# Kernel optimization log

Measured on AMD Instinct MI355X. Metric: run time of the kernel, lower is better.

Reference implementation:

```python
import jax, jax.numpy as jnp
import numpy as np

EPS = 1e-5

def mean_variance_norm(x):
    # x: [b,c,h,w]; torch .var(dim=2) on flattened spatial is UNBIASED (n-1)
    b, c, h, w = x.shape
    n = h * w
    mean = jnp.mean(x, axis=(2, 3), keepdims=True)
    var = jnp.sum((x - mean) ** 2, axis=(2, 3), keepdims=True) / (n - 1) + EPS
    return (x - mean) / jnp.sqrt(var)

def conv1x1(x, W, b):
    # 1x1 conv == channel-mixing matmul. W: [out_c, in_c], b: [out_c]
    return jnp.einsum('oc,bchw->bohw', W, x) + b[None, :, None, None]

def setup_inputs() -> dict:
    key = jax.random.key(0)
    ks = jax.random.split(key, 10)
    C = 512
    shp = (4, C, 64, 64)
    std = 1.0 / np.sqrt(C)
    return {
        'content': jax.random.normal(ks[0], shp, jnp.float32),
        'style': jax.random.normal(ks[1], shp, jnp.float32),
        'Wf': jax.random.normal(ks[2], (C, C), jnp.float32) * std,
        'bf': jax.random.normal(ks[3], (C,), jnp.float32) * 0.01,
        'Wg': jax.random.normal(ks[4], (C, C), jnp.float32) * std,
        'bg': jax.random.normal(ks[5], (C,), jnp.float32) * 0.01,
        'Wh': jax.random.normal(ks[6], (C, C), jnp.float32) * std,
        'bh': jax.random.normal(ks[7], (C,), jnp.float32) * 0.01,
        'Wo': jax.random.normal(ks[8], (C, C), jnp.float32) * std,
        'bo': jax.random.normal(ks[9], (C,), jnp.float32) * 0.01,
    }

def reference(content, style, Wf, bf, Wg, bg, Wh, bh, Wo, bo):
    b, c, h, w = content.shape
    hw = h * w
    F = conv1x1(mean_variance_norm(content), Wf, bf).reshape(b, c, hw)  # queries
    G = conv1x1(mean_variance_norm(style), Wg, bg).reshape(b, c, hw)    # keys
    H = conv1x1(style, Wh, bh).reshape(b, c, hw)                        # values
    # S[b,n,m] = sum_c F[b,c,n] * G[b,c,m]  (unscaled attention scores)
    S = jnp.einsum('bcn,bcm->bnm', F, G)
    S = jax.nn.softmax(S, axis=-1)
    # O[b,c,n] = sum_m H[b,c,m] * S[b,n,m]
    O = jnp.einsum('bcm,bnm->bcn', H, S).reshape(b, c, h, w)
    O = conv1x1(O, Wo, bo)
    return O + content
```

## Files before the change

kernel.cpp:

```cpp
#include <hip/hip_runtime.h>

#define C 512
#define HW 4096
#define EPSV 1e-5f

typedef _Float16 fp16x8 __attribute__((ext_vector_type(8)));
typedef _Float16 fp16x4 __attribute__((ext_vector_type(4)));
typedef float f32x4 __attribute__((ext_vector_type(4)));

#define OFF_MC    (0)
#define OFF_RC    (8192)
#define OFF_MS    (16384)
#define OFF_RS    (24576)
#define OFF_BETAF (32768)
#define OFF_V     (40960)
#define OFF_BZ    (49152)
#define OFF_T     (65536)
#define OFF_SP    (131072)
#define OFF_A     (OFF_SP + 2097152)
#define OFF_WZ    (OFF_A + 1048576)
#define OFF_XCT   (OFF_WZ + 1048576)
#define OFF_XST   (OFF_XCT + 16777216)
#define OFF_KT    (OFF_XST + 16777216)
#define OFF_HM    (OFF_KT + 16777216)
#define OFF_ML    (OFF_HM + 16777216)
#define OFF_S     (OFF_ML + 8388608)

#define FT_IDX(n, c) ((((size_t)((n) >> 4) * 16 + ((c) >> 5)) * 512) + \
                      ((((c) >> 3) & 3) * 128) + (((n) & 15) * 8) + ((c) & 7))

#define SFT_IDX(n, m) ((((size_t)((n) >> 4) * 128 + ((m) >> 5)) * 512) + \
                       ((((m) >> 3) & 3) * 128) + (((n) & 15) * 8) + ((m) & 7))


__global__ void transpose_stats_kernel(const float* __restrict__ xc, const float* __restrict__ xs,
                                       char* __restrict__ ws)
{
    int bx = blockIdx.x;
    int tensor = bx >> 11, b = (bx >> 9) & 3, c0 = ((bx >> 6) & 7) * 64, n0 = (bx & 63) * 64;
    const float* src = tensor ? xs : xc;
    _Float16* dst = (_Float16*)(ws + (tensor ? OFF_XST : OFF_XCT));
    float2* part = (float2*)(ws + OFF_SP);

    __shared__ _Float16 tile[64][72];
    __shared__ float sred[4][64], ssred[4][64];

    int tid = threadIdx.x, cR = tid & 63, ng = tid >> 6;
    const float* p = src + ((size_t)(b * C + c0 + cR)) * HW + n0 + ng * 16;
    float s = 0.f, ss = 0.f;
    #pragma unroll
    for (int k = 0; k < 4; k++) {
        float4 v = *(const float4*)(p + k * 4);
        s += v.x + v.y + v.z + v.w;
        ss += v.x * v.x + v.y * v.y + v.z * v.z + v.w * v.w;
        int n = ng * 16 + k * 4;
        tile[n][cR] = (_Float16)v.x; tile[n + 1][cR] = (_Float16)v.y;
        tile[n + 2][cR] = (_Float16)v.z; tile[n + 3][cR] = (_Float16)v.w;
    }
    sred[ng][cR] = s; ssred[ng][cR] = ss;
    __syncthreads();
    if (tid < 64) {
        float S = sred[0][tid] + sred[1][tid] + sred[2][tid] + sred[3][tid];
        float SS = ssred[0][tid] + ssred[1][tid] + ssred[2][tid] + ssred[3][tid];
        part[((size_t)((tensor * 4 + b) * 512 + c0 + tid)) * 64 + (n0 >> 6)] = make_float2(S, SS);
    }
    _Float16* dstB = dst + (size_t)b * HW * C;
    #pragma unroll
    for (int i = 0; i < 2; i++) {
        int g = tid + i * 256, row = g >> 3, c8 = (g & 7) * 8;
        int n = n0 + row, c = c0 + c8;
        *(fp16x8*)&dstB[FT_IDX(n, c)] = *(const fp16x8*)&tile[row][c8];
    }
}

__global__ void finalize_stats_kernel(char* __restrict__ ws)
{
    int ch = blockIdx.x * 256 + threadIdx.x;
    const float2* part = (const float2*)(ws + OFF_SP) + (size_t)ch * 64;
    float S = 0.f, SS = 0.f;
    for (int k = 0; k < 64; k++) { float2 v = part[k]; S += v.x; SS += v.y; }
    int tensor = ch >> 11, rem = ch & 2047;
    float m = S / (float)HW;
    float var = (SS - S * m) / (float)(HW - 1) + EPSV;
    ((float*)(ws + (tensor ? OFF_MS : OFF_MC)))[rem] = m;
    ((float*)(ws + (tensor ? OFF_RS : OFF_RC)))[rem] = rsqrtf(var);
}

__global__ void precompute_kernel(const float* __restrict__ Wf, const float* __restrict__ Wg,
                                  const float* __restrict__ Wo, const float* __restrict__ Wh,
                                  const float* __restrict__ bf, const float* __restrict__ bh,
                                  char* __restrict__ ws)
{
    float* A = (float*)(ws + OFF_A);
    float* Wz = (float*)(ws + OFF_WZ);
    float* betaf = (float*)(ws + OFF_BETAF);
    float* bz = (float*)(ws + OFF_BZ);
    const float* mc = (const float*)(ws + OFF_MC);
    const float* rc = (const float*)(ws + OFF_RC);
    int bx = blockIdx.x, t = threadIdx.x;
    if (bx < 512) {
        bool isA = bx < 256;
        int r0 = (isA ? bx : bx - 256) * 2;
        float a00 = 0.f, a01 = 0.f, a10 = 0.f, a11 = 0.f;
        for (int k = 0; k < C; k++) {
            float r0v, r1v, c0v, c1v;
            if (isA) {
                r0v = Wf[k * C + r0]; r1v = Wf[k * C + r0 + 1];
                c0v = Wg[k * C + t];  c1v = Wg[k * C + t + 256];
            } else {
                r0v = Wo[r0 * C + k]; r1v = Wo[(r0 + 1) * C + k];
                c0v = Wh[k * C + t];  c1v = Wh[k * C + t + 256];
            }
            a00 += r0v * c0v; a01 += r0v * c1v;
            a10 += r1v * c0v; a11 += r1v * c1v;
        }
        float* D = isA ? A : Wz;
        D[r0 * C + t] = a00;       D[r0 * C + t + 256] = a01;
        D[(r0 + 1) * C + t] = a10; D[(r0 + 1) * C + t + 256] = a11;
    } else if (bx < 520) {
        int g = (bx - 512) * 256 + t, b = g >> 9, co = g & 511;
        float acc = 0.f;
        for (int i = 0; i < C; i++) acc += Wf[co * C + i] * mc[b * C + i] * rc[b * C + i];
        betaf[g] = bf[co] - acc;
    } else {
        int co = (bx - 520) * 256 + t;
        float acc = 0.f;
        for (int i = 0; i < C; i++) acc += Wo[co * C + i] * bh[i];
        bz[co] = acc;
    }
}

__global__ void precompute_v_kernel(const float* __restrict__ Wg, char* __restrict__ ws)
{
    const float* betaf = (const float*)(ws + OFF_BETAF);
    const float* rs = (const float*)(ws + OFF_RS);
    float* v = (float*)(ws + OFF_V);
    int g = blockIdx.x * 32 + (threadIdx.x >> 3);
    int b = g >> 9, j = g & 511, cq = threadIdx.x & 7;
    float acc = 0.f;
    for (int co = cq * 64; co < cq * 64 + 64; co++) acc += betaf[b * C + co] * Wg[co * C + j];
    acc += __shfl_xor(acc, 1);
    acc += __shfl_xor(acc, 2);
    acc += __shfl_xor(acc, 4);
    if (cq == 0) v[g] = rs[b * C + j] * acc;
}

__global__ void __launch_bounds__(256) prep_gemm_kernel(char* __restrict__ ws)
{
    const float* A = (const float*)(ws + OFF_A);
    const float* Wz = (const float*)(ws + OFF_WZ);
    const float* rc = (const float*)(ws + OFF_RC);
    const float* rs = (const float*)(ws + OFF_RS);
    const float* bz = (const float*)(ws + OFF_BZ);
    const _Float16* __restrict__ xsT = (const _Float16*)(ws + OFF_XST);
    _Float16* __restrict__ Kt = (_Float16*)(ws + OFF_KT);
    _Float16* __restrict__ Hp = (_Float16*)(ws + OFF_HM);

    int bx = blockIdx.x;
    int b = bx & 3, rest = bx >> 2;
    int r128 = rest >> 5, mb = rest & 31;
    int r0 = r128 * 128, m0 = mb * 128;
    int w = threadIdx.x >> 6, lane = threadIdx.x & 63, q = lane >> 4, l16 = lane & 15;
    int wr = (w & 1) * 64, wm = (w >> 1) * 64;
    bool isK = (r0 < 512);
    const float* Asrc = isK ? A : Wz;
    int rbase = (isK ? r0 : r0 - 512) + wr;

    f32x4 zz = {0.f, 0.f, 0.f, 0.f};
    f32x4 acc[4][4];
    #pragma unroll
    for (int rt = 0; rt < 4; rt++)
        #pragma unroll
        for (int mt = 0; mt < 4; mt++) acc[rt][mt] = zz;

    float rcv[4];
    #pragma unroll
    for (int rt = 0; rt < 4; rt++)
        rcv[rt] = isK ? rc[b * C + rbase + rt * 16 + l16] : 1.f;

    const _Float16* xb = xsT + (size_t)b * HW * C
                             + (size_t)((m0 + wm) >> 4) * 8192 + q * 128 + l16 * 8;

    for (int ks = 0; ks < 16; ks++) {
        int j0 = ks * 32 + q * 8;
        float rsv[8];
        if (isK) {
            float4 u0 = *(const float4*)&rs[b * C + j0];
            float4 u1 = *(const float4*)&rs[b * C + j0 + 4];
            rsv[0] = u0.x; rsv[1] = u0.y; rsv[2] = u0.z; rsv[3] = u0.w;
            rsv[4] = u1.x; rsv[5] = u1.y; rsv[6] = u1.z; rsv[7] = u1.w;
        } else {
            #pragma unroll
            for (int jj = 0; jj < 8; jj++) rsv[jj] = 1.f;
        }
        fp16x8 afr[4];
        #pragma unroll
        for (int rt = 0; rt < 4; rt++) {
            int row = rbase + rt * 16 + l16;
            float4 a0 = *(const float4*)&Asrc[row * C + j0];
            float4 a1 = *(const float4*)&Asrc[row * C + j0 + 4];
            float av8[8];
            av8[0] = a0.x; av8[1] = a0.y; av8[2] = a0.z; av8[3] = a0.w;
            av8[4] = a1.x; av8[5] = a1.y; av8[6] = a1.z; av8[7] = a1.w;
            float sc = rcv[rt];
            #pragma unroll
            for (int jj = 0; jj < 8; jj++)
                afr[rt][jj] = (_Float16)(isK ? av8[jj] * sc * rsv[jj] : av8[jj]);
        }
        fp16x8 bfr[4];
        #pragma unroll
        for (int mt = 0; mt < 4; mt++)
            bfr[mt] = *(const fp16x8*)(xb + (size_t)(mt * 16 + ks) * 512);
        #pragma unroll
        for (int rt = 0; rt < 4; rt++)
            #pragma unroll
            for (int mt = 0; mt < 4; mt++)
                acc[rt][mt] = __builtin_amdgcn_mfma_f32_16x16x32_f16(afr[rt], bfr[mt], acc[rt][mt], 0, 0, 0);
    }

    if (isK) {
        _Float16* KtB = Kt + (size_t)b * HW * C;
        #pragma unroll
        for (int rt = 0; rt < 4; rt++)
            #pragma unroll
            for (int mt = 0; mt < 4; mt++) {
                int m = m0 + wm + mt * 16 + l16;
                int cb = r0 + wr + rt * 16 + q * 4;
                fp16x4 h;
                h[0] = (_Float16)acc[rt][mt][0]; h[1] = (_Float16)acc[rt][mt][1];
                h[2] = (_Float16)acc[rt][mt][2]; h[3] = (_Float16)acc[rt][mt][3];
                *(fp16x4*)&KtB[FT_IDX(m, cb)] = h;
            }
    } else {
        _Float16* HpB = Hp + (size_t)b * 2097152;
        #pragma unroll
        for (int rt = 0; rt < 4; rt++) {
            float bzv[4];
            #pragma unroll
            for (int reg = 0; reg < 4; reg++) bzv[reg] = bz[rbase + rt * 16 + q * 4 + reg];
            #pragma unroll
            for (int mt = 0; mt < 4; mt++) {
                int m = m0 + wm + mt * 16 + l16;
                int mbase = (m >> 3) * 128 + (m & 7);
                #pragma unroll
                for (int reg = 0; reg < 4; reg++) {
                    int co = rbase + rt * 16 + q * 4 + reg;
                    HpB[(size_t)(co >> 4) * 65536 + mbase + (co & 15) * 8] =
                        (_Float16)(acc[rt][mt][reg] + bzv[reg]);
                }
            }
        }
    }
}

__global__ void t_kernel(char* __restrict__ ws)
{
    const float* v = (const float*)(ws + OFF_V);
    const _Float16* __restrict__ xsT = (const _Float16*)(ws + OFF_XST);
    float* tG = (float*)(ws + OFF_T);
    int bx = blockIdx.x;
    int b = bx >> 7, m0 = (bx & 127) * 32;
    int m = m0 + (threadIdx.x >> 3), cq = threadIdx.x & 7;
    const _Float16* p = xsT + (size_t)b * HW * C + (size_t)(m >> 4) * 8192 + (m & 15) * 8;
    const float* vp = v + b * C + cq * 64;
    float acc = 0.f;
    #pragma unroll
    for (int k = 0; k < 8; k++) {
        fp16x8 xv = *(const fp16x8*)(p + (cq * 2 + (k >> 2)) * 512 + (k & 3) * 128);
        float4 v0 = *(const float4*)(vp + k * 8);
        float4 v1 = *(const float4*)(vp + k * 8 + 4);
        acc += (float)xv[0] * v0.x + (float)xv[1] * v0.y + (float)xv[2] * v0.z + (float)xv[3] * v0.w
             + (float)xv[4] * v1.x + (float)xv[5] * v1.y + (float)xv[6] * v1.z + (float)xv[7] * v1.w;
    }
    acc += __shfl_xor(acc, 1);
    acc += __shfl_xor(acc, 2);
    acc += __shfl_xor(acc, 4);
    if (cq == 0) tG[b * HW + m] = acc;
}

__global__ void __launch_bounds__(256, 4) qk_kernel(char* __restrict__ ws)
{
    const _Float16* __restrict__ xcT = (const _Float16*)(ws + OFF_XCT);
    const _Float16* __restrict__ Kt = (const _Float16*)(ws + OFF_KT);
    const float* __restrict__ tG = (const float*)(ws + OFF_T);
    float2* __restrict__ ML = (float2*)(ws + OFF_ML);
    _Float16* __restrict__ Sg = (_Float16*)(ws + OFF_S);

    int bx = blockIdx.x;
    int b = (bx >> 1) & 3, mhi = bx & 1;
    int rest = bx >> 3, mlo = rest & 15, ntile = rest >> 4;
    int m0 = (mhi * 16 + mlo) * 128, n0 = ntile * 128;
    int tid = threadIdx.x, w = tid >> 6, lane = tid & 63, q = lane >> 4, l16 = lane & 15;
    int wn = (w & 1) * 64, wm = (w >> 1) * 64;

    const _Float16* ab = xcT + (size_t)b * HW * C
                             + (size_t)((n0 + wn) >> 4) * 8192 + q * 128 + l16 * 8;
    const _Float16* bb = Kt + (size_t)b * HW * C
                            + (size_t)((m0 + wm) >> 4) * 8192 + q * 128 + l16 * 8;

    f32x4 zz = {0.f, 0.f, 0.f, 0.f};
    f32x4 acc[4][4];
    #pragma unroll
    for (int nt = 0; nt < 4; nt++)
        #pragma unroll
        for (int mt = 0; mt < 4; mt++) acc[nt][mt] = zz;

    #pragma unroll 4
    for (int ks = 0; ks < 16; ks++) {
        fp16x8 afr[4], bfr[4];
        #pragma unroll
        for (int nt = 0; nt < 4; nt++)
            afr[nt] = *(const fp16x8*)(ab + (size_t)(nt * 16 + ks) * 512);
        #pragma unroll
        for (int mt = 0; mt < 4; mt++)
            bfr[mt] = *(const fp16x8*)(bb + (size_t)(mt * 16 + ks) * 512);
        #pragma unroll
        for (int nt = 0; nt < 4; nt++)
            #pragma unroll
            for (int mt = 0; mt < 4; mt++)
                acc[nt][mt] = __builtin_amdgcn_mfma_f32_16x16x32_f16(afr[nt], bfr[mt], acc[nt][mt], 0, 0, 0);
    }

    float tv[4];
    #pragma unroll
    for (int mt = 0; mt < 4; mt++) tv[mt] = tG[b * HW + m0 + wm + mt * 16 + l16];
    #pragma unroll
    for (int nt = 0; nt < 4; nt++)
        #pragma unroll
        for (int mt = 0; mt < 4; mt++)
            #pragma unroll
            for (int reg = 0; reg < 4; reg++) acc[nt][mt][reg] += tv[mt];

    float rm[4][4], sum[4][4];
    #pragma unroll
    for (int nt = 0; nt < 4; nt++)
        #pragma unroll
        for (int reg = 0; reg < 4; reg++)
            rm[nt][reg] = fmaxf(fmaxf(acc[nt][0][reg], acc[nt][1][reg]),
                                fmaxf(acc[nt][2][reg], acc[nt][3][reg]));
    #pragma unroll
    for (int s = 1; s < 16; s <<= 1)
        #pragma unroll
        for (int nt = 0; nt < 4; nt++)
            #pragma unroll
            for (int reg = 0; reg < 4; reg++)
                rm[nt][reg] = fmaxf(rm[nt][reg], __shfl_xor(rm[nt][reg], s));
    #pragma unroll
    for (int nt = 0; nt < 4; nt++)
        #pragma unroll
        for (int reg = 0; reg < 4; reg++) sum[nt][reg] = 0.f;
    #pragma unroll
    for (int nt = 0; nt < 4; nt++)
        #pragma unroll
        for (int mt = 0; mt < 4; mt++)
            #pragma unroll
            for (int reg = 0; reg < 4; reg++) {
                float pv = __expf(acc[nt][mt][reg] - rm[nt][reg]);
                acc[nt][mt][reg] = pv;
                sum[nt][reg] += pv;
            }
    #pragma unroll
    for (int s = 1; s < 16; s <<= 1)
        #pragma unroll
        for (int nt = 0; nt < 4; nt++)
            #pragma unroll
            for (int reg = 0; reg < 4; reg++)
                sum[nt][reg] += __shfl_xor(sum[nt][reg], s);

    int tl = (m0 + wm) >> 6;
    if (l16 == 0) {
        #pragma unroll
        for (int nt = 0; nt < 4; nt++)
            #pragma unroll
            for (int reg = 0; reg < 4; reg++)
                ML[((size_t)(b * HW + n0 + wn + nt * 16 + q * 4 + reg)) * 64 + tl] =
                    make_float2(rm[nt][reg], sum[nt][reg]);
    }

    __shared__ _Float16 Pl[4][64][72];
    #pragma unroll
    for (int nt = 0; nt < 4; nt++)
        #pragma unroll
        for (int mt = 0; mt < 4; mt++)
            #pragma unroll
            for (int reg = 0; reg < 4; reg++)
                Pl[w][nt * 16 + q * 4 + reg][mt * 16 + l16] = (_Float16)acc[nt][mt][reg];
    __syncthreads();
    _Float16* SgB = Sg + (size_t)b * 16777216;
    #pragma unroll
    for (int i = 0; i < 8; i++) {
        int row = i * 8 + (lane >> 3), c8 = (lane & 7) * 8;
        int n = n0 + wn + row, m = m0 + wm + c8;
        *(fp16x8*)&SgB[SFT_IDX(n, m)] = *(const fp16x8*)&Pl[w][row][c8];
    }
}

__global__ void scale_kernel(char* __restrict__ ws)
{
    const float2* __restrict__ ML = (const float2*)(ws + OFF_ML);
    float* __restrict__ Scl = (float*)(ws + OFF_XCT);
    int g = blockIdx.x * 128 + threadIdx.x;
    const float2* mlp = ML + (size_t)g * 64;
    float M = -1e30f;
    #pragma unroll
    for (int k = 0; k < 64; k += 4) {
        float4 a = *(const float4*)(mlp + k);
        float4 c = *(const float4*)(mlp + k + 2);
        M = fmaxf(M, fmaxf(fmaxf(a.x, a.z), fmaxf(c.x, c.z)));
    }
    float L = 0.f;
    #pragma unroll
    for (int k = 0; k < 64; k += 2) {
        float4 a = *(const float4*)(mlp + k);
        L += a.y * __expf(a.x - M) + a.w * __expf(a.z - M);
    }
    float linv = 1.f / L;
    int b = g >> 12, n = g & 4095;
    float* sp = Scl + (size_t)b * 262144 + n;
    #pragma unroll
    for (int k = 0; k < 64; k += 2) {
        float4 a = *(const float4*)(mlp + k);
        sp[(size_t)k * 4096] = __expf(a.x - M) * linv;
        sp[(size_t)(k + 1) * 4096] = __expf(a.z - M) * linv;
    }
}

__global__ void __launch_bounds__(512) pv_kernel(const float* __restrict__ xc,
                                                 const float* __restrict__ bo,
                                                 float* __restrict__ out,
                                                 char* __restrict__ ws)
{
    const _Float16* __restrict__ Sft = (const _Float16*)(ws + OFF_S);
    const _Float16* __restrict__ Hp = (const _Float16*)(ws + OFF_HM);
    const float* __restrict__ Scl = (const float*)(ws + OFF_XCT);

    int bx = blockIdx.x;
    int b = bx & 3, ntile = bx >> 2;
    int n0 = ntile * 32;
    int tid = threadIdx.x, w = tid >> 6, lane = tid & 63, q = lane >> 4, l16 = lane & 15;
    int co0 = w * 64;

    const _Float16* sb = Sft + (size_t)b * 16777216
                             + (size_t)(ntile * 2) * 65536 + q * 128 + l16 * 8;
    const _Float16* hb = Hp + (size_t)b * 2097152 + (size_t)(co0 >> 4) * 65536
                            + q * 128 + l16 * 8;
    const float* sc = Scl + (size_t)b * 262144 + n0 + q * 4;

    f32x4 zz = {0.f, 0.f, 0.f, 0.f};
    f32x4 acc[2][4];
    #pragma unroll
    for (int nt = 0; nt < 2; nt++)
        #pragma unroll
        for (int ct = 0; ct < 4; ct++) acc[nt][ct] = zz;

    for (int chunk = 0; chunk < 64; chunk++) {
        fp16x8 afr[2][2], bfr[2][4];
        #pragma unroll
        for (int km = 0; km < 2; km++) {
            #pragma unroll
            for (int nt = 0; nt < 2; nt++)
                afr[km][nt] = *(const fp16x8*)(sb + (size_t)nt * 65536 + (chunk * 2 + km) * 512);
            #pragma unroll
            for (int ct = 0; ct < 4; ct++)
                bfr[km][ct] = *(const fp16x8*)(hb + (size_t)ct * 65536 + (chunk * 8 + km * 4) * 128);
        }
        float4 sv0 = *(const float4*)(sc + chunk * 4096);
        float4 sv1 = *(const float4*)(sc + chunk * 4096 + 16);

        f32x4 tmp[2][4];
        #pragma unroll
        for (int km = 0; km < 2; km++)
            #pragma unroll
            for (int nt = 0; nt < 2; nt++)
                #pragma unroll
                for (int ct = 0; ct < 4; ct++)
                    tmp[nt][ct] = __builtin_amdgcn_mfma_f32_16x16x32_f16(
                        afr[km][nt], bfr[km][ct], km == 0 ? zz : tmp[nt][ct], 0, 0, 0);

        float sva[2][4] = {{sv0.x, sv0.y, sv0.z, sv0.w}, {sv1.x, sv1.y, sv1.z, sv1.w}};
        #pragma unroll
        for (int nt = 0; nt < 2; nt++)
            #pragma unroll
            for (int ct = 0; ct < 4; ct++)
                #pragma unroll
                for (int reg = 0; reg < 4; reg++)
                    acc[nt][ct][reg] += tmp[nt][ct][reg] * sva[nt][reg];
    }

    #pragma unroll
    for (int nt = 0; nt < 2; nt++)
        #pragma unroll
        for (int ct = 0; ct < 4; ct++) {
            int co = co0 + ct * 16 + l16;
            size_t base = ((size_t)(b * C + co)) * HW + n0 + nt * 16 + q * 4;
            float4 cv = *(const float4*)&xc[base];
            float bov = bo[co];
            float4 o;
            o.x = acc[nt][ct][0] + bov + cv.x;
            o.y = acc[nt][ct][1] + bov + cv.y;
            o.z = acc[nt][ct][2] + bov + cv.z;
            o.w = acc[nt][ct][3] + bov + cv.w;
            *(float4*)&out[base] = o;
        }
}

extern "C" void kernel_launch(void* const* d_in, const int* in_sizes, int n_in,
                              void* d_out, int out_size, void* d_ws, size_t ws_size,
                              hipStream_t stream)
{
    const float* content = (const float*)d_in[0];
    const float* style   = (const float*)d_in[1];
    const float* Wf = (const float*)d_in[2];
    const float* bf = (const float*)d_in[3];
    const float* Wg = (const float*)d_in[4];
    const float* Wh = (const float*)d_in[6];
    const float* bh = (const float*)d_in[7];
    const float* Wo = (const float*)d_in[8];
    const float* bo = (const float*)d_in[9];
    float* out = (float*)d_out;
    char* ws = (char*)d_ws;

    transpose_stats_kernel<<<4096, 256, 0, stream>>>(content, style, ws);
    finalize_stats_kernel<<<16, 256, 0, stream>>>(ws);
    precompute_kernel<<<522, 256, 0, stream>>>(Wf, Wg, Wo, Wh, bf, bh, ws);
    precompute_v_kernel<<<64, 256, 0, stream>>>(Wg, ws);
    prep_gemm_kernel<<<1024, 256, 0, stream>>>(ws);
    t_kernel<<<512, 256, 0, stream>>>(ws);
    qk_kernel<<<4096, 256, 0, stream>>>(ws);
    scale_kernel<<<128, 128, 0, stream>>>(ws);
    pv_kernel<<<512, 512, 0, stream>>>(content, bo, out, ws);
}
```

Before: 550.9 us.

## Stage shared H tile in LDS for PV kernel, restructure scale kernel

The PV kernel is remapped so each 256-thread block covers one 64-channel output group across 128 positions, with four waves sharing an H tile. That tile is double-buffered in LDS and prefetched one chunk ahead. The scale kernel now loads the max/sum partials through shared memory in 64-row blocks and writes coalesced along n instead of with strided per-thread stores. This cuts redundant global H reads and uncoalesced writes, but adds a barrier on every chunk and changes the grid and occupancy.

After: 506.8 us. 8.0% less time.

```diff
diff --git a/kernel.cpp b/kernel.cpp
--- a/kernel.cpp
+++ b/kernel.cpp
@@ -395,56 +395,77 @@
     }
 }
 
-__global__ void scale_kernel(char* __restrict__ ws)
-{
-    const float2* __restrict__ ML = (const float2*)(ws + OFF_ML);
+__global__ void __launch_bounds__(256) scale_kernel(char* __restrict__ ws)
+{
+    const float* __restrict__ mlf0 = (const float*)(ws + OFF_ML);
     float* __restrict__ Scl = (float*)(ws + OFF_XCT);
-    int g = blockIdx.x * 128 + threadIdx.x;
-    const float2* mlp = ML + (size_t)g * 64;
-    float M = -1e30f;
-    #pragma unroll
-    for (int k = 0; k < 64; k += 4) {
-        float4 a = *(const float4*)(mlp + k);
-        float4 c = *(const float4*)(mlp + k + 2);
-        M = fmaxf(M, fmaxf(fmaxf(a.x, a.z), fmaxf(c.x, c.z)));
-    }
-    float L = 0.f;
-    #pragma unroll
-    for (int k = 0; k < 64; k += 2) {
-        float4 a = *(const float4*)(mlp + k);
-        L += a.y * __expf(a.x - M) + a.w * __expf(a.z - M);
-    }
-    float linv = 1.f / L;
-    int b = g >> 12, n = g & 4095;
-    float* sp = Scl + (size_t)b * 262144 + n;
-    #pragma unroll
-    for (int k = 0; k < 64; k += 2) {
-        float4 a = *(const float4*)(mlp + k);
-        sp[(size_t)k * 4096] = __expf(a.x - M) * linv;
-        sp[(size_t)(k + 1) * 4096] = __expf(a.z - M) * linv;
-    }
-}
-
-__global__ void __launch_bounds__(512) pv_kernel(const float* __restrict__ xc,
-                                                 const float* __restrict__ bo,
-                                                 float* __restrict__ out,
-                                                 char* __restrict__ ws)
+    __shared__ float mlv[64][129];
+    __shared__ float Ms[64], Li[64];
+
+    int g0 = blockIdx.x * 64;
+    int tid = threadIdx.x;
+    const float* mlf = mlf0 + (size_t)g0 * 128;
+
+    #pragma unroll
+    for (int i = 0; i < 8; i++) {
+        int f4 = i * 256 + tid;
+        int row = f4 >> 5, c4 = (f4 & 31) * 4;
+        float4 v = *(const float4*)(mlf + row * 128 + c4);
+        mlv[row][c4] = v.x; mlv[row][c4 + 1] = v.y;
+        mlv[row][c4 + 2] = v.z; mlv[row][c4 + 3] = v.w;
+    }
+    __syncthreads();
+    if (tid < 64) {
+        float M = -1e30f;
+        #pragma unroll
+        for (int k = 0; k < 64; k++) M = fmaxf(M, mlv[tid][k * 2]);
+        float L = 0.f;
+        #pragma unroll
+        for (int k = 0; k < 64; k++) L += mlv[tid][k * 2 + 1] * __expf(mlv[tid][k * 2] - M);
+        Ms[tid] = M; Li[tid] = 1.f / L;
+    }
+    __syncthreads();
+    int b = g0 >> 12, nbase = g0 & 4095;
+    float* sp = Scl + (size_t)b * 262144 + nbase;
+    int row = tid & 63, tsub = tid >> 6;
+    #pragma unroll
+    for (int pass = 0; pass < 16; pass++) {
+        int tile = pass * 4 + tsub;
+        sp[(size_t)tile * 4096 + row] = __expf(mlv[row][tile * 2] - Ms[row]) * Li[row];
+    }
+}
+
+__global__ void __launch_bounds__(256, 4) pv_kernel(const float* __restrict__ xc,
+                                                    const float* __restrict__ bo,
+                                                    float* __restrict__ out,
+                                                    char* __restrict__ ws)
 {
     const _Float16* __restrict__ Sft = (const _Float16*)(ws + OFF_S);
     const _Float16* __restrict__ Hp = (const _Float16*)(ws + OFF_HM);
     const float* __restrict__ Scl = (const float*)(ws + OFF_XCT);
 
     int bx = blockIdx.x;
-    int b = bx & 3, ntile = bx >> 2;
-    int n0 = ntile * 32;
+    int b = bx & 3, cog = (bx >> 2) & 7, ntb = bx >> 5;
+    int co0 = cog * 64;
     int tid = threadIdx.x, w = tid >> 6, lane = tid & 63, q = lane >> 4, l16 = lane & 15;
-    int co0 = w * 64;
-
+    int n0w = ntb * 128 + w * 32;
+
+    __shared__ _Float16 Hl[2][4096];
+
+    int ln64 = lane;
+    const _Float16* hsrc = Hp + (size_t)b * 2097152
+                              + (size_t)((co0 >> 4) + w) * 65536 + ln64 * 8;
     const _Float16* sb = Sft + (size_t)b * 16777216
-                             + (size_t)(ntile * 2) * 65536 + q * 128 + l16 * 8;
-    const _Float16* hb = Hp + (size_t)b * 2097152 + (size_t)(co0 >> 4) * 65536
-                            + q * 128 + l16 * 8;
-    const float* sc = Scl + (size_t)b * 262144 + n0 + q * 4;
+                             + (size_t)(ntb * 8 + w * 2) * 65536 + q * 128 + l16 * 8;
+    const float* sc = Scl + (size_t)b * 262144 + n0w + q * 4;
+
+    {
+        fp16x8 s0 = *(const fp16x8*)(hsrc);
+        fp16x8 s1 = *(const fp16x8*)(hsrc + 512);
+        *(fp16x8*)&Hl[0][w * 1024 + ln64 * 8] = s0;
+        *(fp16x8*)&Hl[0][w * 1024 + 512 + ln64 * 8] = s1;
+    }
+    __syncthreads();
 
     f32x4 zz = {0.f, 0.f, 0.f, 0.f};
     f32x4 acc[2][4];
@@ -454,29 +475,32 @@
         for (int ct = 0; ct < 4; ct++) acc[nt][ct] = zz;
 
     for (int chunk = 0; chunk < 64; chunk++) {
-        fp16x8 afr[2][2], bfr[2][4];
+        int buf = chunk & 1;
+        fp16x8 s0n, s1n;
+        if (chunk < 63) {
+            s0n = *(const fp16x8*)(hsrc + (chunk + 1) * 1024);
+            s1n = *(const fp16x8*)(hsrc + (chunk + 1) * 1024 + 512);
+        }
+
+        f32x4 tmp[2][4];
         #pragma unroll
         for (int km = 0; km < 2; km++) {
+            fp16x8 afr[2], bfr[4];
             #pragma unroll
             for (int nt = 0; nt < 2; nt++)
-                afr[km][nt] = *(const fp16x8*)(sb + (size_t)nt * 65536 + (chunk * 2 + km) * 512);
+                afr[nt] = *(const fp16x8*)(sb + (size_t)nt * 65536 + (chunk * 2 + km) * 512);
             #pragma unroll
             for (int ct = 0; ct < 4; ct++)
-                bfr[km][ct] = *(const fp16x8*)(hb + (size_t)ct * 65536 + (chunk * 8 + km * 4) * 128);
-        }
-        float4 sv0 = *(const float4*)(sc + chunk * 4096);
-        float4 sv1 = *(const float4*)(sc + chunk * 4096 + 16);
-
-        f32x4 tmp[2][4];
-        #pragma unroll
-        for (int km = 0; km < 2; km++)
+                bfr[ct] = *(const fp16x8*)&Hl[buf][ct * 1024 + (km * 4 + q) * 128 + l16 * 8];
             #pragma unroll
             for (int nt = 0; nt < 2; nt++)
                 #pragma unroll
                 for (int ct = 0; ct < 4; ct++)
                     tmp[nt][ct] = __builtin_amdgcn_mfma_f32_16x16x32_f16(
-                        afr[km][nt], bfr[km][ct], km == 0 ? zz : tmp[nt][ct], 0, 0, 0);
-
+                        afr[nt], bfr[ct], km == 0 ? zz : tmp[nt][ct], 0, 0, 0);
+        }
+        float4 sv0 = *(const float4*)(sc + chunk * 4096);
+        float4 sv1 = *(const float4*)(sc + chunk * 4096 + 16);
         float sva[2][4] = {{sv0.x, sv0.y, sv0.z, sv0.w}, {sv1.x, sv1.y, sv1.z, sv1.w}};
         #pragma unroll
         for (int nt = 0; nt < 2; nt++)
@@ -485,6 +509,12 @@
                 #pragma unroll
                 for (int reg = 0; reg < 4; reg++)
                     acc[nt][ct][reg] += tmp[nt][ct][reg] * sva[nt][reg];
+
+        if (chunk < 63) {
+            *(fp16x8*)&Hl[buf ^ 1][w * 1024 + ln64 * 8] = s0n;
+            *(fp16x8*)&Hl[buf ^ 1][w * 1024 + 512 + ln64 * 8] = s1n;
+        }
+        __syncthreads();
     }
 
     #pragma unroll
@@ -492,7 +522,7 @@
         #pragma unroll
         for (int ct = 0; ct < 4; ct++) {
             int co = co0 + ct * 16 + l16;
-            size_t base = ((size_t)(b * C + co)) * HW + n0 + nt * 16 + q * 4;
+            size_t base = ((size_t)(b * C + co)) * HW + n0w + nt * 16 + q * 4;
             float4 cv = *(const float4*)&xc[base];
             float bov = bo[co];
             float4 o;
@@ -527,6 +557,6 @@
     prep_gemm_kernel<<<1024, 256, 0, stream>>>(ws);
     t_kernel<<<512, 256, 0, stream>>>(ws);
     qk_kernel<<<4096, 256, 0, stream>>>(ws);
-    scale_kernel<<<128, 128, 0, stream>>>(ws);
-    pv_kernel<<<512, 512, 0, stream>>>(content, bo, out, ws);
-}
+    scale_kernel<<<256, 256, 0, stream>>>(ws);
+    pv_kernel<<<1024, 256, 0, stream>>>(content, bo, out, ws);
+}
```
